# Performance work log

Hardware: AMD Instinct MI355X
Metric: run time of the kernel (lower is better)

Reference implementation:

```python
import jax, jax.numpy as jnp
import numpy as np

B, E, K = 512, 4096, 1024      # batch, emb_dim, key_dim
M, L = 1024, 32                # mem_size, prompt_length
TOP_K = 4
EPS = 1e-12


def _l2norm(x, axis=-1):
    n = jnp.linalg.norm(x, axis=axis, keepdims=True)
    return x / jnp.maximum(n, EPS)


def setup_inputs() -> dict:
    key = jax.random.key(0)
    k1, k2, k3, k4 = jax.random.split(key, 4)
    return {
        "x_query": jax.random.normal(k1, (B, E), dtype=jnp.float32),
        "W_proj": jax.random.normal(k2, (K, E), dtype=jnp.float32) * 0.02,
        "prompt_memory": jax.random.normal(k3, (M, L, E), dtype=jnp.float32) * 0.02,
        "prompt_keys": jax.random.normal(k4, (M, K), dtype=jnp.float32) * 0.02,
        "top_k": TOP_K,
    }


def reference(x_query, W_proj, prompt_memory, prompt_keys, top_k):
    # x_proj = Linear(emb_dim -> key_dim, no bias): x @ W.T
    x_proj = jnp.einsum("be,ke->bk", x_query, W_proj)          # [B, K]
    x_norm = _l2norm(x_proj)                                     # [B, K]
    key_norm = _l2norm(prompt_keys)                              # [M, K]
    sim = jnp.einsum("bk,mk->bm", x_norm, key_norm)             # [B, M]
    _, idx = jax.lax.top_k(sim, top_k)                           # [B, top_k]
    sel_prompts = prompt_memory[idx]                             # [B, top_k, L, E]
    sel_keys = _l2norm(prompt_keys[idx], axis=2)                 # [B, top_k, K]
    refined = jnp.einsum("bk,btk->bt", x_norm, sel_keys)        # [B, top_k]
    w = jax.nn.softmax(refined, axis=1)                          # [B, top_k]
    # softmax-weighted sum over selected prompts
    out = jnp.einsum("btle,bt->ble", sel_prompts, w)            # [B, L, E]
    return out
```

## Files before the change

kernel.cpp:

```cpp
#include <hip/hip_runtime.h>
#include <math.h>

#define BDIM 512
#define EDIM 4096
#define KDIM 1024
#define MDIM 1024
#define LDIM 32
#define TOPK 4
#define EPSF 1e-12f

typedef __attribute__((ext_vector_type(8))) short short8;
typedef __attribute__((ext_vector_type(4))) float f32x4;

struct us4 { ushort x, y, z, w; };

__device__ inline ushort f2bf_rn(float x) {
    union { float f; unsigned u; } v; v.f = x;
    unsigned r = (v.u + 0x7FFF + ((v.u >> 16) & 1)) >> 16;
    return (ushort)r;
}
__device__ inline float bf2f(ushort h) {
    union { unsigned u; float f; } v; v.u = ((unsigned)h) << 16;
    return v.f;
}

__global__ __launch_bounds__(256)
void split_all_kernel(const float* __restrict__ xq, const float* __restrict__ wp,
                      const float* __restrict__ pk,
                      ushort* __restrict__ xq_h, ushort* __restrict__ xq_l,
                      ushort* __restrict__ wp_h, ushort* __restrict__ wp_l,
                      ushort* __restrict__ pk_h, ushort* __restrict__ pk_l,
                      float* __restrict__ kn)
{
    const int blk = blockIdx.x;
    const int t = threadIdx.x;
    const float* src; ushort* hi; ushort* lo; int base;
    bool do_norm = false; int rowbase = 0;
    if (blk < 512)       { src = xq; hi = xq_h; lo = xq_l; base = blk * 1024; }
    else if (blk < 1536) { src = wp; hi = wp_h; lo = wp_l; base = (blk - 512) * 1024; }
    else                 { src = pk; hi = pk_h; lo = pk_l; base = (blk - 1536) * 1024;
                           do_norm = true; rowbase = (blk - 1536) * 4; }

    __shared__ float wsum[4];
    const int lane = t & 63, wwid = t >> 6;

    #pragma unroll
    for (int it = 0; it < 4; ++it) {
        const int i = base + it * 256 + t;
        float4 v = ((const float4*)src)[i];
        us4 h, l;
        h.x = f2bf_rn(v.x); l.x = f2bf_rn(v.x - bf2f(h.x));
        h.y = f2bf_rn(v.y); l.y = f2bf_rn(v.y - bf2f(h.y));
        h.z = f2bf_rn(v.z); l.z = f2bf_rn(v.z - bf2f(h.z));
        h.w = f2bf_rn(v.w); l.w = f2bf_rn(v.w - bf2f(h.w));
        ((us4*)hi)[i] = h;
        ((us4*)lo)[i] = l;

        if (do_norm) {
            float sq = v.x * v.x + v.y * v.y + v.z * v.z + v.w * v.w;
            #pragma unroll
            for (int off = 32; off > 0; off >>= 1) sq += __shfl_down(sq, off, 64);
            __syncthreads();
            if (lane == 0) wsum[wwid] = sq;
            __syncthreads();
            if (t == 0)
                kn[rowbase + it] = sqrtf(wsum[0] + wsum[1] + wsum[2] + wsum[3]);
        }
    }
}

__global__ __launch_bounds__(256)
void gemm1_kernel(const ushort* __restrict__ Ah, const ushort* __restrict__ Al,
                  const ushort* __restrict__ Bh, const ushort* __restrict__ Bl,
                  float* __restrict__ Cp)
{
    __shared__ ushort ldsA[2][64][40];
    __shared__ ushort ldsB[2][128][40];

    const int t  = threadIdx.x;
    const int bn = blockIdx.x, bm = blockIdx.y, kz = blockIdx.z;
    const int srow = t >> 2, sg = t & 3;
    const int Kc = EDIM / 4;

    const size_t aoff  = (size_t)(bm * 64 + srow) * EDIM + kz * Kc + sg * 8;
    const size_t boff0 = (size_t)(bn * 128 + srow) * EDIM + kz * Kc + sg * 8;
    const size_t boff1 = (size_t)(bn * 128 + 64 + srow) * EDIM + kz * Kc + sg * 8;

    const int lane = t & 63, wid = t >> 6;
    const int wr = wid >> 1, wc = wid & 1;
    const int fr = lane & 15, fg = lane >> 4;

    f32x4 acc[2][4];
    #pragma unroll
    for (int i = 0; i < 2; ++i)
        #pragma unroll
        for (int j = 0; j < 4; ++j)
            acc[i][j] = (f32x4){0.f, 0.f, 0.f, 0.f};

    short8 pAh = *(const short8*)(Ah + aoff);
    short8 pAl = *(const short8*)(Al + aoff);
    short8 pBh0 = *(const short8*)(Bh + boff0);
    short8 pBl0 = *(const short8*)(Bl + boff0);
    short8 pBh1 = *(const short8*)(Bh + boff1);
    short8 pBl1 = *(const short8*)(Bl + boff1);

    for (int k0 = 0; k0 < Kc; k0 += 32) {
        *(short8*)(&ldsA[0][srow][sg * 8]) = pAh;
        *(short8*)(&ldsA[1][srow][sg * 8]) = pAl;
        *(short8*)(&ldsB[0][srow][sg * 8]) = pBh0;
        *(short8*)(&ldsB[1][srow][sg * 8]) = pBl0;
        *(short8*)(&ldsB[0][64 + srow][sg * 8]) = pBh1;
        *(short8*)(&ldsB[1][64 + srow][sg * 8]) = pBl1;
        __syncthreads();

        if (k0 + 32 < Kc) {
            pAh = *(const short8*)(Ah + aoff + k0 + 32);
            pAl = *(const short8*)(Al + aoff + k0 + 32);
            pBh0 = *(const short8*)(Bh + boff0 + k0 + 32);
            pBl0 = *(const short8*)(Bl + boff0 + k0 + 32);
            pBh1 = *(const short8*)(Bh + boff1 + k0 + 32);
            pBl1 = *(const short8*)(Bl + boff1 + k0 + 32);
        }

        short8 ah[2], al[2], bh[4], bl[4];
        #pragma unroll
        for (int i = 0; i < 2; ++i) {
            ah[i] = *(const short8*)(&ldsA[0][wr * 32 + i * 16 + fr][fg * 8]);
            al[i] = *(const short8*)(&ldsA[1][wr * 32 + i * 16 + fr][fg * 8]);
        }
        #pragma unroll
        for (int j = 0; j < 4; ++j) {
            bh[j] = *(const short8*)(&ldsB[0][wc * 64 + j * 16 + fr][fg * 8]);
            bl[j] = *(const short8*)(&ldsB[1][wc * 64 + j * 16 + fr][fg * 8]);
        }
        #pragma unroll
        for (int i = 0; i < 2; ++i)
            #pragma unroll
            for (int j = 0; j < 4; ++j) {
                acc[i][j] = __builtin_amdgcn_mfma_f32_16x16x32_bf16(ah[i], bh[j], acc[i][j], 0, 0, 0);
                acc[i][j] = __builtin_amdgcn_mfma_f32_16x16x32_bf16(ah[i], bl[j], acc[i][j], 0, 0, 0);
                acc[i][j] = __builtin_amdgcn_mfma_f32_16x16x32_bf16(al[i], bh[j], acc[i][j], 0, 0, 0);
            }
        __syncthreads();
    }

    float* Cz = Cp + (size_t)kz * BDIM * KDIM;
    #pragma unroll
    for (int i = 0; i < 2; ++i)
        #pragma unroll
        for (int j = 0; j < 4; ++j)
            #pragma unroll
            for (int q = 0; q < 4; ++q) {
                int orow = bm * 64 + wr * 32 + i * 16 + (lane >> 4) * 4 + q;
                int ocol = bn * 128 + wc * 64 + j * 16 + (lane & 15);
                Cz[(size_t)orow * KDIM + ocol] = acc[i][j][q];
            }
}

__global__ __launch_bounds__(256)
void gemm_mfma_split(const ushort* __restrict__ Ah, const ushort* __restrict__ Al,
                     const ushort* __restrict__ Bh, const ushort* __restrict__ Bl,
                     float* __restrict__ Cp, int M, int N, int K, int Kchunk)
{
    __shared__ ushort lds[4][64][40];

    const int t  = threadIdx.x;
    const int bn = blockIdx.x, bm = blockIdx.y, kz = blockIdx.z;

    const int srow = t >> 2, sg = t & 3;
    const size_t aoff = (size_t)(bm * 64 + srow) * K + sg * 8 + (size_t)kz * Kchunk;
    const size_t boff = (size_t)(bn * 64 + srow) * K + sg * 8 + (size_t)kz * Kchunk;

    const int lane = t & 63, wid = t >> 6;
    const int wr = wid >> 1, wc = wid & 1;
    const int fr = lane & 15, fg = lane >> 4;

    f32x4 acc[2][2];
    #pragma unroll
    for (int i = 0; i < 2; ++i)
        #pragma unroll
        for (int j = 0; j < 2; ++j)
            acc[i][j] = (f32x4){0.f, 0.f, 0.f, 0.f};

    short8 pA0 = *(const short8*)(Ah + aoff);
    short8 pA1 = *(const short8*)(Al + aoff);
    short8 pB0 = *(const short8*)(Bh + boff);
    short8 pB1 = *(const short8*)(Bl + boff);

    for (int k0 = 0; k0 < Kchunk; k0 += 32) {
        *(short8*)(&lds[0][srow][sg * 8]) = pA0;
        *(short8*)(&lds[1][srow][sg * 8]) = pA1;
        *(short8*)(&lds[2][srow][sg * 8]) = pB0;
        *(short8*)(&lds[3][srow][sg * 8]) = pB1;
        __syncthreads();

        if (k0 + 32 < Kchunk) {
            pA0 = *(const short8*)(Ah + aoff + k0 + 32);
            pA1 = *(const short8*)(Al + aoff + k0 + 32);
            pB0 = *(const short8*)(Bh + boff + k0 + 32);
            pB1 = *(const short8*)(Bl + boff + k0 + 32);
        }

        short8 ah[2], al[2], bh[2], bl[2];
        #pragma unroll
        for (int i = 0; i < 2; ++i) {
            ah[i] = *(const short8*)(&lds[0][wr * 32 + i * 16 + fr][fg * 8]);
            al[i] = *(const short8*)(&lds[1][wr * 32 + i * 16 + fr][fg * 8]);
            bh[i] = *(const short8*)(&lds[2][wc * 32 + i * 16 + fr][fg * 8]);
            bl[i] = *(const short8*)(&lds[3][wc * 32 + i * 16 + fr][fg * 8]);
        }
        #pragma unroll
        for (int i = 0; i < 2; ++i)
            #pragma unroll
            for (int j = 0; j < 2; ++j) {
                acc[i][j] = __builtin_amdgcn_mfma_f32_16x16x32_bf16(ah[i], bh[j], acc[i][j], 0, 0, 0);
                acc[i][j] = __builtin_amdgcn_mfma_f32_16x16x32_bf16(ah[i], bl[j], acc[i][j], 0, 0, 0);
                acc[i][j] = __builtin_amdgcn_mfma_f32_16x16x32_bf16(al[i], bh[j], acc[i][j], 0, 0, 0);
            }
        __syncthreads();
    }

    float* Cz = Cp + (size_t)kz * M * N;
    #pragma unroll
    for (int i = 0; i < 2; ++i)
        #pragma unroll
        for (int j = 0; j < 2; ++j)
            #pragma unroll
            for (int q = 0; q < 4; ++q) {
                int orow = bm * 64 + wr * 32 + i * 16 + (lane >> 4) * 4 + q;
                int ocol = bn * 64 + wc * 32 + j * 16 + (lane & 15);
                Cz[(size_t)orow * N + ocol] = acc[i][j][q];
            }
}

__global__ __launch_bounds__(256)
void reduce_split_norm_kernel(const float* __restrict__ Cp,
                              ushort* __restrict__ xh, ushort* __restrict__ xl,
                              float* __restrict__ xn)
{
    const int b = blockIdx.x;
    const int i = b * 256 + threadIdx.x;
    const int n4 = BDIM * KDIM / 4;

    float4 s = ((const float4*)Cp)[i];
    #pragma unroll
    for (int z = 1; z < 4; ++z) {
        float4 v = ((const float4*)Cp)[(size_t)z * n4 + i];
        s.x += v.x; s.y += v.y; s.z += v.z; s.w += v.w;
    }

    us4 h, l;
    h.x = f2bf_rn(s.x); l.x = f2bf_rn(s.x - bf2f(h.x));
    h.y = f2bf_rn(s.y); l.y = f2bf_rn(s.y - bf2f(h.y));
    h.z = f2bf_rn(s.z); l.z = f2bf_rn(s.z - bf2f(h.z));
    h.w = f2bf_rn(s.w); l.w = f2bf_rn(s.w - bf2f(h.w));
    ((us4*)xh)[i] = h;
    ((us4*)xl)[i] = l;

    float sq = s.x * s.x + s.y * s.y + s.z * s.z + s.w * s.w;
    #pragma unroll
    for (int off = 32; off > 0; off >>= 1) sq += __shfl_down(sq, off, 64);
    __shared__ float wsum[4];
    const int lane = threadIdx.x & 63, wwid = threadIdx.x >> 6;
    if (lane == 0) wsum[wwid] = sq;
    __syncthreads();
    if (threadIdx.x == 0)
        xn[b] = sqrtf(wsum[0] + wsum[1] + wsum[2] + wsum[3]);
}

__device__ inline bool tk_better(float x, int ix, float y, int iy) {
    return (x > y) || (x == y && ix < iy);
}
__device__ inline void tk_insert(float (&v)[4], int (&id)[4], float x, int m) {
    if (tk_better(x, m, v[3], id[3])) {
        v[3] = x; id[3] = m;
        if (tk_better(v[3], id[3], v[2], id[2])) {
            float tv = v[2]; int ti = id[2]; v[2] = v[3]; id[2] = id[3]; v[3] = tv; id[3] = ti;
            if (tk_better(v[2], id[2], v[1], id[1])) {
                tv = v[1]; ti = id[1]; v[1] = v[2]; id[1] = id[2]; v[2] = tv; id[2] = ti;
                if (tk_better(v[1], id[1], v[0], id[0])) {
                    tv = v[0]; ti = id[0]; v[0] = v[1]; id[0] = id[1]; v[1] = tv; id[1] = ti;
                }
            }
        }
    }
}
__global__ __launch_bounds__(64)
void topk_scale_kernel(const float* __restrict__ Cp2, const float* __restrict__ xn,
                       const float* __restrict__ kn,
                       int* __restrict__ topi, float* __restrict__ topw)
{
    const int b = blockIdx.x;
    const int lane = threadIdx.x;
    const float sb = 1.f / fmaxf(xn[b], EPSF);
    const float* r0 = Cp2 + (size_t)b * MDIM;
    const float* r1 = Cp2 + (size_t)BDIM * MDIM + (size_t)b * MDIM;

    float v[4] = {-INFINITY, -INFINITY, -INFINITY, -INFINITY};
    int id[4] = {-1, -1, -1, -1};
    for (int j = 0; j < MDIM / 64; ++j) {
        int m = j * 64 + lane;
        float s = (r0[m] + r1[m]) * sb / fmaxf(kn[m], EPSF);
        tk_insert(v, id, s, m);
    }
    for (int off = 32; off >= 1; off >>= 1) {
        float pv[4]; int pi[4];
        #pragma unroll
        for (int q = 0; q < 4; ++q) {
            pv[q] = __shfl_xor(v[q], off, 64);
            pi[q] = __shfl_xor(id[q], off, 64);
        }
        #pragma unroll
        for (int q = 0; q < 4; ++q) tk_insert(v, id, pv[q], pi[q]);
    }
    if (lane == 0) {
        const float mx = fmaxf(fmaxf(v[0], v[1]), fmaxf(v[2], v[3]));
        const float e0 = expf(v[0] - mx), e1 = expf(v[1] - mx);
        const float e2 = expf(v[2] - mx), e3 = expf(v[3] - mx);
        const float inv = 1.f / (e0 + e1 + e2 + e3);
        topw[b * 4 + 0] = e0 * inv; topw[b * 4 + 1] = e1 * inv;
        topw[b * 4 + 2] = e2 * inv; topw[b * 4 + 3] = e3 * inv;
        #pragma unroll
        for (int q = 0; q < 4; ++q) topi[b * 4 + q] = id[q];
    }
}

__global__ __launch_bounds__(256)
void gather_out_kernel(const float* __restrict__ pm, const int* __restrict__ topi,
                       const float* __restrict__ topw, float* __restrict__ out)
{
    const int bl = blockIdx.x;
    const int b = bl & (BDIM - 1);
    const int l = bl >> 9;

    const int j0 = topi[b * 4 + 0], j1 = topi[b * 4 + 1], j2 = topi[b * 4 + 2], j3 = topi[b * 4 + 3];
    const float w0 = topw[b * 4 + 0], w1 = topw[b * 4 + 1], w2 = topw[b * 4 + 2], w3 = topw[b * 4 + 3];

    const f32x4* p0 = (const f32x4*)(pm + ((size_t)j0 * LDIM + l) * EDIM);
    const f32x4* p1 = (const f32x4*)(pm + ((size_t)j1 * LDIM + l) * EDIM);
    const f32x4* p2 = (const f32x4*)(pm + ((size_t)j2 * LDIM + l) * EDIM);
    const f32x4* p3 = (const f32x4*)(pm + ((size_t)j3 * LDIM + l) * EDIM);
    f32x4* o = (f32x4*)(out + ((size_t)b * LDIM + l) * EDIM);

    for (int c = threadIdx.x; c < EDIM / 4; c += 256) {
        f32x4 a = p0[c], bb = p1[c], cc = p2[c], dd = p3[c];
        f32x4 r = w0 * a + w1 * bb + w2 * cc + w3 * dd;
        __builtin_nontemporal_store(r, &o[c]);
    }
}

extern "C" void kernel_launch(void* const* d_in, const int* in_sizes, int n_in,
                              void* d_out, int out_size, void* d_ws, size_t ws_size,
                              hipStream_t stream)
{
    const float* x_query = (const float*)d_in[0];
    const float* W_proj  = (const float*)d_in[1];
    const float* pm      = (const float*)d_in[2];
    const float* pkeys   = (const float*)d_in[3];
    float* out = (float*)d_out;

    char* w = (char*)d_ws;
    ushort* xq_h = (ushort*)w; w += (size_t)BDIM * EDIM * 2;
    ushort* xq_l = (ushort*)w; w += (size_t)BDIM * EDIM * 2;
    ushort* wp_h = (ushort*)w; w += (size_t)KDIM * EDIM * 2;
    ushort* wp_l = (ushort*)w; w += (size_t)KDIM * EDIM * 2;
    ushort* pk_h = (ushort*)w; w += (size_t)MDIM * KDIM * 2;
    ushort* pk_l = (ushort*)w; w += (size_t)MDIM * KDIM * 2;
    ushort* xp_h = (ushort*)w; w += (size_t)BDIM * KDIM * 2;
    ushort* xp_l = (ushort*)w; w += (size_t)BDIM * KDIM * 2;
    float* Cp1  = (float*)w; w += (size_t)4 * BDIM * KDIM * 4;
    float* Cp2  = (float*)w; w += (size_t)2 * BDIM * MDIM * 4;
    float* xn   = (float*)w; w += BDIM * 4;
    float* kn   = (float*)w; w += MDIM * 4;
    float* topw = (float*)w; w += BDIM * TOPK * 4;
    int*   topi = (int*)w;   w += BDIM * TOPK * 4;

    split_all_kernel<<<1792, 256, 0, stream>>>(
        x_query, W_proj, pkeys, xq_h, xq_l, wp_h, wp_l, pk_h, pk_l, kn);

    gemm1_kernel<<<dim3(KDIM / 128, BDIM / 64, 4), 256, 0, stream>>>(
        xq_h, xq_l, wp_h, wp_l, Cp1);

    reduce_split_norm_kernel<<<BDIM, 256, 0, stream>>>(Cp1, xp_h, xp_l, xn);

    gemm_mfma_split<<<dim3(MDIM / 64, BDIM / 64, 2), 256, 0, stream>>>(
        xp_h, xp_l, pk_h, pk_l, Cp2, BDIM, MDIM, KDIM, KDIM / 2);

    topk_scale_kernel<<<BDIM, 64, 0, stream>>>(Cp2, xn, kn, topi, topw);

    gather_out_kernel<<<BDIM * LDIM, 256, 0, stream>>>(pm, topi, topw, out);
}
```

Measured before the change: 236.5 us.

## Double-buffer LDS in both GEMMs, widen top-k block, unroll gather loop

```diff
diff --git a/kernel.cpp b/kernel.cpp
--- a/kernel.cpp
+++ b/kernel.cpp
@@ -74,8 +74,8 @@
                   const ushort* __restrict__ Bh, const ushort* __restrict__ Bl,
                   float* __restrict__ Cp)
 {
-    __shared__ ushort ldsA[2][64][40];
-    __shared__ ushort ldsB[2][128][40];
+    __shared__ ushort ldsA[2][2][64][40];
+    __shared__ ushort ldsB[2][2][128][40];
 
     const int t  = threadIdx.x;
     const int bn = blockIdx.x, bm = blockIdx.y, kz = blockIdx.z;
@@ -104,16 +104,17 @@
     short8 pBh1 = *(const short8*)(Bh + boff1);
     short8 pBl1 = *(const short8*)(Bl + boff1);
 
+    *(short8*)(&ldsA[0][0][srow][sg * 8]) = pAh;
+    *(short8*)(&ldsA[0][1][srow][sg * 8]) = pAl;
+    *(short8*)(&ldsB[0][0][srow][sg * 8]) = pBh0;
+    *(short8*)(&ldsB[0][1][srow][sg * 8]) = pBl0;
+    *(short8*)(&ldsB[0][0][64 + srow][sg * 8]) = pBh1;
+    *(short8*)(&ldsB[0][1][64 + srow][sg * 8]) = pBl1;
+
+    int p = 0;
     for (int k0 = 0; k0 < Kc; k0 += 32) {
-        *(short8*)(&ldsA[0][srow][sg * 8]) = pAh;
-        *(short8*)(&ldsA[1][srow][sg * 8]) = pAl;
-        *(short8*)(&ldsB[0][srow][sg * 8]) = pBh0;
-        *(short8*)(&ldsB[1][srow][sg * 8]) = pBl0;
-        *(short8*)(&ldsB[0][64 + srow][sg * 8]) = pBh1;
-        *(short8*)(&ldsB[1][64 + srow][sg * 8]) = pBl1;
-        __syncthreads();
-
-        if (k0 + 32 < Kc) {
+        const bool more = (k0 + 32 < Kc);
+        if (more) {
             pAh = *(const short8*)(Ah + aoff + k0 + 32);
             pAl = *(const short8*)(Al + aoff + k0 + 32);
             pBh0 = *(const short8*)(Bh + boff0 + k0 + 32);
@@ -121,17 +122,18 @@
             pBh1 = *(const short8*)(Bh + boff1 + k0 + 32);
             pBl1 = *(const short8*)(Bl + boff1 + k0 + 32);
         }
+        __syncthreads();
 
         short8 ah[2], al[2], bh[4], bl[4];
         #pragma unroll
         for (int i = 0; i < 2; ++i) {
-            ah[i] = *(const short8*)(&ldsA[0][wr * 32 + i * 16 + fr][fg * 8]);
-            al[i] = *(const short8*)(&ldsA[1][wr * 32 + i * 16 + fr][fg * 8]);
+            ah[i] = *(const short8*)(&ldsA[p][0][wr * 32 + i * 16 + fr][fg * 8]);
+            al[i] = *(const short8*)(&ldsA[p][1][wr * 32 + i * 16 + fr][fg * 8]);
         }
         #pragma unroll
         for (int j = 0; j < 4; ++j) {
-            bh[j] = *(const short8*)(&ldsB[0][wc * 64 + j * 16 + fr][fg * 8]);
-            bl[j] = *(const short8*)(&ldsB[1][wc * 64 + j * 16 + fr][fg * 8]);
+            bh[j] = *(const short8*)(&ldsB[p][0][wc * 64 + j * 16 + fr][fg * 8]);
+            bl[j] = *(const short8*)(&ldsB[p][1][wc * 64 + j * 16 + fr][fg * 8]);
         }
         #pragma unroll
         for (int i = 0; i < 2; ++i)
@@ -141,7 +143,16 @@
                 acc[i][j] = __builtin_amdgcn_mfma_f32_16x16x32_bf16(ah[i], bl[j], acc[i][j], 0, 0, 0);
                 acc[i][j] = __builtin_amdgcn_mfma_f32_16x16x32_bf16(al[i], bh[j], acc[i][j], 0, 0, 0);
             }
-        __syncthreads();
+
+        if (more) {
+            *(short8*)(&ldsA[p ^ 1][0][srow][sg * 8]) = pAh;
+            *(short8*)(&ldsA[p ^ 1][1][srow][sg * 8]) = pAl;
+            *(short8*)(&ldsB[p ^ 1][0][srow][sg * 8]) = pBh0;
+            *(short8*)(&ldsB[p ^ 1][1][srow][sg * 8]) = pBl0;
+            *(short8*)(&ldsB[p ^ 1][0][64 + srow][sg * 8]) = pBh1;
+            *(short8*)(&ldsB[p ^ 1][1][64 + srow][sg * 8]) = pBl1;
+        }
+        p ^= 1;
     }
 
     float* Cz = Cp + (size_t)kz * BDIM * KDIM;
@@ -158,18 +169,19 @@
 }
 
 __global__ __launch_bounds__(256)
-void gemm_mfma_split(const ushort* __restrict__ Ah, const ushort* __restrict__ Al,
-                     const ushort* __restrict__ Bh, const ushort* __restrict__ Bl,
-                     float* __restrict__ Cp, int M, int N, int K, int Kchunk)
-{
-    __shared__ ushort lds[4][64][40];
+void gemm2_kernel(const ushort* __restrict__ Ah, const ushort* __restrict__ Al,
+                  const ushort* __restrict__ Bh, const ushort* __restrict__ Bl,
+                  float* __restrict__ Cp)
+{
+    __shared__ ushort lds[2][4][64][40];
 
     const int t  = threadIdx.x;
     const int bn = blockIdx.x, bm = blockIdx.y, kz = blockIdx.z;
-
     const int srow = t >> 2, sg = t & 3;
-    const size_t aoff = (size_t)(bm * 64 + srow) * K + sg * 8 + (size_t)kz * Kchunk;
-    const size_t boff = (size_t)(bn * 64 + srow) * K + sg * 8 + (size_t)kz * Kchunk;
+    const int Kc = KDIM / 2;
+
+    const size_t aoff = (size_t)(bm * 64 + srow) * KDIM + kz * Kc + sg * 8;
+    const size_t boff = (size_t)(bn * 64 + srow) * KDIM + kz * Kc + sg * 8;
 
     const int lane = t & 63, wid = t >> 6;
     const int wr = wid >> 1, wc = wid & 1;
@@ -187,27 +199,29 @@
     short8 pB0 = *(const short8*)(Bh + boff);
     short8 pB1 = *(const short8*)(Bl + boff);
 
-    for (int k0 = 0; k0 < Kchunk; k0 += 32) {
-        *(short8*)(&lds[0][srow][sg * 8]) = pA0;
-        *(short8*)(&lds[1][srow][sg * 8]) = pA1;
-        *(short8*)(&lds[2][srow][sg * 8]) = pB0;
-        *(short8*)(&lds[3][srow][sg * 8]) = pB1;
-        __syncthreads();
-
-        if (k0 + 32 < Kchunk) {
+    *(short8*)(&lds[0][0][srow][sg * 8]) = pA0;
+    *(short8*)(&lds[0][1][srow][sg * 8]) = pA1;
+    *(short8*)(&lds[0][2][srow][sg * 8]) = pB0;
+    *(short8*)(&lds[0][3][srow][sg * 8]) = pB1;
+
+    int p = 0;
+    for (int k0 = 0; k0 < Kc; k0 += 32) {
+        const bool more = (k0 + 32 < Kc);
+        if (more) {
             pA0 = *(const short8*)(Ah + aoff + k0 + 32);
             pA1 = *(const short8*)(Al + aoff + k0 + 32);
             pB0 = *(const short8*)(Bh + boff + k0 + 32);
             pB1 = *(const short8*)(Bl + boff + k0 + 32);
         }
+        __syncthreads();
 
         short8 ah[2], al[2], bh[2], bl[2];
         #pragma unroll
         for (int i = 0; i < 2; ++i) {
-            ah[i] = *(const short8*)(&lds[0][wr * 32 + i * 16 + fr][fg * 8]);
-            al[i] = *(const short8*)(&lds[1][wr * 32 + i * 16 + fr][fg * 8]);
-            bh[i] = *(const short8*)(&lds[2][wc * 32 + i * 16 + fr][fg * 8]);
-            bl[i] = *(const short8*)(&lds[3][wc * 32 + i * 16 + fr][fg * 8]);
+            ah[i] = *(const short8*)(&lds[p][0][wr * 32 + i * 16 + fr][fg * 8]);
+            al[i] = *(const short8*)(&lds[p][1][wr * 32 + i * 16 + fr][fg * 8]);
+            bh[i] = *(const short8*)(&lds[p][2][wc * 32 + i * 16 + fr][fg * 8]);
+            bl[i] = *(const short8*)(&lds[p][3][wc * 32 + i * 16 + fr][fg * 8]);
         }
         #pragma unroll
         for (int i = 0; i < 2; ++i)
@@ -217,10 +231,17 @@
                 acc[i][j] = __builtin_amdgcn_mfma_f32_16x16x32_bf16(ah[i], bl[j], acc[i][j], 0, 0, 0);
                 acc[i][j] = __builtin_amdgcn_mfma_f32_16x16x32_bf16(al[i], bh[j], acc[i][j], 0, 0, 0);
             }
-        __syncthreads();
-    }
-
-    float* Cz = Cp + (size_t)kz * M * N;
+
+        if (more) {
+            *(short8*)(&lds[p ^ 1][0][srow][sg * 8]) = pA0;
+            *(short8*)(&lds[p ^ 1][1][srow][sg * 8]) = pA1;
+            *(short8*)(&lds[p ^ 1][2][srow][sg * 8]) = pB0;
+            *(short8*)(&lds[p ^ 1][3][srow][sg * 8]) = pB1;
+        }
+        p ^= 1;
+    }
+
+    float* Cz = Cp + (size_t)kz * BDIM * MDIM;
     #pragma unroll
     for (int i = 0; i < 2; ++i)
         #pragma unroll
@@ -229,7 +250,7 @@
             for (int q = 0; q < 4; ++q) {
                 int orow = bm * 64 + wr * 32 + i * 16 + (lane >> 4) * 4 + q;
                 int ocol = bn * 64 + wc * 32 + j * 16 + (lane & 15);
-                Cz[(size_t)orow * N + ocol] = acc[i][j][q];
+                Cz[(size_t)orow * MDIM + ocol] = acc[i][j][q];
             }
 }
 
@@ -285,21 +306,22 @@
         }
     }
 }
-__global__ __launch_bounds__(64)
+__global__ __launch_bounds__(256)
 void topk_scale_kernel(const float* __restrict__ Cp2, const float* __restrict__ xn,
                        const float* __restrict__ kn,
                        int* __restrict__ topi, float* __restrict__ topw)
 {
-    const int b = blockIdx.x;
-    const int lane = threadIdx.x;
+    const int b = blockIdx.x, t = threadIdx.x;
+    const int lane = t & 63, wid = t >> 6;
     const float sb = 1.f / fmaxf(xn[b], EPSF);
     const float* r0 = Cp2 + (size_t)b * MDIM;
     const float* r1 = Cp2 + (size_t)BDIM * MDIM + (size_t)b * MDIM;
 
     float v[4] = {-INFINITY, -INFINITY, -INFINITY, -INFINITY};
     int id[4] = {-1, -1, -1, -1};
-    for (int j = 0; j < MDIM / 64; ++j) {
-        int m = j * 64 + lane;
+    #pragma unroll
+    for (int j = 0; j < MDIM / 256; ++j) {
+        int m = wid * 256 + j * 64 + lane;
         float s = (r0[m] + r1[m]) * sb / fmaxf(kn[m], EPSF);
         tk_insert(v, id, s, m);
     }
@@ -313,15 +335,31 @@
         #pragma unroll
         for (int q = 0; q < 4; ++q) tk_insert(v, id, pv[q], pi[q]);
     }
+
+    __shared__ float sv[4][4];
+    __shared__ int   si[4][4];
     if (lane == 0) {
-        const float mx = fmaxf(fmaxf(v[0], v[1]), fmaxf(v[2], v[3]));
-        const float e0 = expf(v[0] - mx), e1 = expf(v[1] - mx);
-        const float e2 = expf(v[2] - mx), e3 = expf(v[3] - mx);
+        #pragma unroll
+        for (int q = 0; q < 4; ++q) { sv[wid][q] = v[q]; si[wid][q] = id[q]; }
+    }
+    __syncthreads();
+    if (t == 0) {
+        float fv[4] = {-INFINITY, -INFINITY, -INFINITY, -INFINITY};
+        int   fi[4] = {-1, -1, -1, -1};
+        #pragma unroll
+        for (int w = 0; w < 4; ++w)
+            #pragma unroll
+            for (int q = 0; q < 4; ++q)
+                tk_insert(fv, fi, sv[w][q], si[w][q]);
+
+        const float mx = fmaxf(fmaxf(fv[0], fv[1]), fmaxf(fv[2], fv[3]));
+        const float e0 = expf(fv[0] - mx), e1 = expf(fv[1] - mx);
+        const float e2 = expf(fv[2] - mx), e3 = expf(fv[3] - mx);
         const float inv = 1.f / (e0 + e1 + e2 + e3);
         topw[b * 4 + 0] = e0 * inv; topw[b * 4 + 1] = e1 * inv;
         topw[b * 4 + 2] = e2 * inv; topw[b * 4 + 3] = e3 * inv;
         #pragma unroll
-        for (int q = 0; q < 4; ++q) topi[b * 4 + q] = id[q];
+        for (int q = 0; q < 4; ++q) topi[b * 4 + q] = fi[q];
     }
 }
 
@@ -342,7 +380,9 @@
     const f32x4* p3 = (const f32x4*)(pm + ((size_t)j3 * LDIM + l) * EDIM);
     f32x4* o = (f32x4*)(out + ((size_t)b * LDIM + l) * EDIM);
 
-    for (int c = threadIdx.x; c < EDIM / 4; c += 256) {
+    #pragma unroll
+    for (int it = 0; it < EDIM / 4 / 256; ++it) {
+        const int c = it * 256 + threadIdx.x;
         f32x4 a = p0[c], bb = p1[c], cc = p2[c], dd = p3[c];
         f32x4 r = w0 * a + w1 * bb + w2 * cc + w3 * dd;
         __builtin_nontemporal_store(r, &o[c]);
@@ -383,10 +423,10 @@
 
     reduce_split_norm_kernel<<<BDIM, 256, 0, stream>>>(Cp1, xp_h, xp_l, xn);
 
-    gemm_mfma_split<<<dim3(MDIM / 64, BDIM / 64, 2), 256, 0, stream>>>(
-        xp_h, xp_l, pk_h, pk_l, Cp2, BDIM, MDIM, KDIM, KDIM / 2);
-
-    topk_scale_kernel<<<BDIM, 64, 0, stream>>>(Cp2, xn, kn, topi, topw);
+    gemm2_kernel<<<dim3(MDIM / 64, BDIM / 64, 2), 256, 0, stream>>>(
+        xp_h, xp_l, pk_h, pk_l, Cp2);
+
+    topk_scale_kernel<<<BDIM, 256, 0, stream>>>(Cp2, xn, kn, topi, topw);
 
     gather_out_kernel<<<BDIM * LDIM, 256, 0, stream>>>(pm, topi, topw, out);
 }
```

After: 234.6 us. About the same (-0.8%).
